# Kernel tuning notes

Hardware: AMD Instinct MI355X
Metric: run time of the kernel (lower is better)

Reference implementation:

```python
import jax, jax.numpy as jnp
import numpy as np

GAMMA = 1.0        # softmin temperature
BANDWIDTH = 0      # 0 => no Sakoe-Chiba band (numba code only skips when 0 < bw < |i-j|)
BIG = 1e30         # finite stand-in for +inf: exp(-BIG/gamma) underflows to exactly 0 in fp32,
                   # reproducing the inf-initialized R/SigR softmin ratios without NaNs
B, N, M = 32, 512, 512


def setup_inputs() -> dict:
    k1, k2 = jax.random.split(jax.random.key(0))
    D = jax.random.uniform(k1, (B, N, M), dtype=jnp.float32)    # pairwise distances (>= 0)
    Sig = jax.random.uniform(k2, (B, N, M), dtype=jnp.float32)  # per-cell uncertainty
    return {"D": D, "Sig": Sig}


def _soft_dtw(D, Sig):
    """uDTW forward DP (compute_softdtw), vectorized over anti-diagonal wavefronts.
    Returns jnp.stack([R[:, N, M], SigR[:, N, M]]) of shape (2, B)."""
    b, n, m = D.shape
    alpha = 1.0 / GAMMA
    # Dp[i, j] == D_new[i, j] = D[i-1, j-1] with zero border (indices 0..N, 0..M)
    Dp = jnp.pad(D, ((0, 0), (1, 0), (1, 0)))
    Sp = jnp.pad(Sig, ((0, 0), (1, 0), (1, 0)))
    iarr = jnp.arange(n + 1)

    def diag(A, d):
        # A[:, i, d - i] for i = 0..N, zero where j out of [0, M]
        j = d - iarr
        vals = A[:, iarr, jnp.clip(j, 0, m)]
        return jnp.where((j >= 0) & (j <= m), vals, 0.0)

    def shift(x, fill):
        # x[:, i-1] (index i-1 along the diagonal buffer)
        return jnp.concatenate([jnp.full((b, 1), fill, x.dtype), x[:, :-1]], axis=1)

    # diagonal buffers indexed by i; diag d=0 holds R[0,0]=0, rest inf(BIG); diag d=1 all inf
    r2 = jnp.full((b, n + 1), BIG, jnp.float32).at[:, 0].set(0.0)
    r1 = jnp.full((b, n + 1), BIG, jnp.float32)
    s2 = jnp.full((b, n + 1), BIG, jnp.float32).at[:, 0].set(0.0)
    s1 = jnp.full((b, n + 1), BIG, jnp.float32)

    def step(carry, d):
        r2, r1, s2, s1 = carry  # R/SigR diagonals d-2 and d-1
        j = d - iarr
        valid = (iarr >= 1) & (j >= 1) & (j <= m)
        if BANDWIDTH > 0:
            valid = valid & (jnp.abs(iarr - j) <= BANDWIDTH)
        # softmin ratios from R neighbors: (i-1,j-1)=prev2 shifted, (i-1,j)=prev1 shifted, (i,j-1)=prev1
        rr0 = -alpha * shift(r2, BIG)
        rr1 = -alpha * shift(r1, BIG)
        rr2 = -alpha * r1
        rmax = jnp.maximum(jnp.maximum(rr0, rr1), rr2)
        e0 = jnp.exp(rr0 - rmax)
        e1 = jnp.exp(rr1 - rmax)
        e2 = jnp.exp(rr2 - rmax)
        inv = 1.0 / (e0 + e1 + e2)
        p0, p1, p2 = e0 * inv, e1 * inv, e2 * inv
        dDd, dD1, dD2 = diag(Dp, d), diag(Dp, d - 1), diag(Dp, d - 2)
        dSd, dS1, dS2 = diag(Sp, d), diag(Sp, d - 1), diag(Sp, d - 2)
        # R[i,j] = D[i-1,j-1] + softmin-weighted avg of D_new neighbors (uDTW recurrence)
        newR = jnp.where(valid, dDd + p0 * shift(dD2, 0.0) + p1 * shift(dD1, 0.0) + p2 * dD1, BIG)
        newS = jnp.where(valid, dSd + p0 * shift(dS2, 0.0) + p1 * shift(dS1, 0.0) + p2 * dS1, BIG)
        return (r1, newR, s1, newS), None

    (_, rlast, _, slast), _ = jax.lax.scan(step, (r2, r1, s2, s1), jnp.arange(2, n + m + 1))
    # last anti-diagonal d = N + M contains cell (N, M) at index i = N
    return jnp.stack([rlast[:, n], slast[:, n]])  # (2, B)


def reference(D, Sig):
    return _soft_dtw(D, Sig)
```

## Files before the change

### kernel.cpp

```cpp
#include <hip/hip_runtime.h>


constexpr int N = 512;
constexpr int M = 512;
constexpr int BATCH = 32;
constexpr int NM = N + M;
constexpr int K = 32;
constexpr int NB = 32;
constexpr int PHASES = NB + 7;
constexpr float NL2E = -1.4426950408889634f;
constexpr float NLN2 = -0.6931471805599453f;
constexpr float EPS  = 1e-30f;

__device__ __forceinline__ float lane_shr1_or(float oldv, float x) {
  return __int_as_float(__builtin_amdgcn_update_dpp(
      __float_as_int(oldv), __float_as_int(x), 0x138, 0xf, 0xf, false));
}
__device__ __forceinline__ int qclamp(int q) {
  return q < 0 ? 0 : (q > 127 ? 127 : q);
}

__global__ __launch_bounds__(512, 2)
void softdtw_fwd(const float* __restrict__ D,
                 const float* __restrict__ Sig,
                 float* __restrict__ out) {
  const int b = blockIdx.x;
  const int t = threadIdx.x;
  const int w = t >> 6;
  const float4* Drow4 = (const float4*)(D + ((size_t)b * N + t) * M);

  __shared__ float2 edge[8][640];
  for (int idx = t; idx < 8 * 640; idx += 512)
    ((float2*)edge)[idx] = make_float2(0.f, 0.f);

  float eSelf = 0.f, dSelfL = 0.f;
  float eN2 = (t == 0) ? 1.f : 0.f, dN2L = 0.f;

  float sgA = 0.f, sg0 = 0.f, sg1 = 0.f, sg2 = 0.f;
  if (t == N - 1) {
    const float* Sb = Sig + (size_t)b * N * M;
    sgA = Sb[(size_t)(N - 1) * M + (M - 1)];
    sg0 = Sb[(size_t)(N - 2) * M + (M - 2)];
    sg1 = Sb[(size_t)(N - 2) * M + (M - 1)];
    sg2 = Sb[(size_t)(N - 1) * M + (M - 2)];
  }

  const int Bl = 2 * w, Bh = 2 * w + 17;

  float4 r0, r1, r2, r3, r4, r5, r6, r7, r8;
  {
    const int q = (32 * Bl - t) >> 2;
    r0 = Drow4[qclamp(q + 0)]; r1 = Drow4[qclamp(q + 1)];
    r2 = Drow4[qclamp(q + 2)]; r3 = Drow4[qclamp(q + 3)];
    r4 = Drow4[qclamp(q + 4)]; r5 = Drow4[qclamp(q + 5)];
    r6 = Drow4[qclamp(q + 6)]; r7 = Drow4[qclamp(q + 7)];
    r8 = Drow4[qclamp(q + 8)];
  }
  __syncthreads();

  for (int p = 0; p < PHASES; ++p) {
    const int B = p - w;
    const int nB = B + 1;
    const bool dopre = (nB >= Bl) && (nB <= Bh);

    float4 p0, p1, p2, p3, p4, p5, p6, p7, p8;
    if (dopre) {
      const int q = (32 * nB - t) >> 2;
      p0 = Drow4[qclamp(q + 0)]; p1 = Drow4[qclamp(q + 1)];
      p2 = Drow4[qclamp(q + 2)]; p3 = Drow4[qclamp(q + 3)];
      p4 = Drow4[qclamp(q + 4)]; p5 = Drow4[qclamp(q + 5)];
      p6 = Drow4[qclamp(q + 6)]; p7 = Drow4[qclamp(q + 7)];
      p8 = Drow4[qclamp(q + 8)];
    }

    if (B >= Bl && B <= Bh) {
      const int d0 = 2 + B * K;
      const int c0 = d0 - t - 2;

      float4 n0, n1, n2, n3, n4, n5, n6, n7, n8, n9, n10, n11, n12, n13, n14, n15;
      if (w > 0) {
        const float4* ep = (const float4*)&edge[w - 1][64 + (d0 - 64 * w - 2)];
        n0 = ep[0];  n1 = ep[1];  n2 = ep[2];  n3 = ep[3];
        n4 = ep[4];  n5 = ep[5];  n6 = ep[6];  n7 = ep[7];
        n8 = ep[8];  n9 = ep[9];  n10 = ep[10]; n11 = ep[11];
        n12 = ep[12]; n13 = ep[13]; n14 = ep[14]; n15 = ep[15];
      } else {
        const float4 z = make_float4(0.f, 0.f, 0.f, 0.f);
        n0 = n1 = n2 = n3 = n4 = n5 = n6 = n7 = z;
        n8 = n9 = n10 = n11 = n12 = n13 = n14 = n15 = z;
      }

      const int s = c0 & 3;
      const bool s2 = (s & 2) != 0, s1b = (s & 1) != 0;
      const float
        f0 = r0.x, f1 = r0.y, f2 = r0.z, f3 = r0.w,
        f4 = r1.x, f5 = r1.y, f6 = r1.z, f7 = r1.w,
        f8 = r2.x, f9 = r2.y, f10 = r2.z, f11 = r2.w,
        f12 = r3.x, f13 = r3.y, f14 = r3.z, f15 = r3.w,
        f16 = r4.x, f17 = r4.y, f18 = r4.z, f19 = r4.w,
        f20 = r5.x, f21 = r5.y, f22 = r5.z, f23 = r5.w,
        f24 = r6.x, f25 = r6.y, f26 = r6.z, f27 = r6.w,
        f28 = r7.x, f29 = r7.y, f30 = r7.z, f31 = r7.w,
        f32 = r8.x, f33 = r8.y, f34 = r8.z, f35 = r8.w;
      const float
        x0  = s2 ? f2  : f0,  x1  = s2 ? f3  : f1,  x2  = s2 ? f4  : f2,
        x3  = s2 ? f5  : f3,  x4  = s2 ? f6  : f4,  x5  = s2 ? f7  : f5,
        x6  = s2 ? f8  : f6,  x7  = s2 ? f9  : f7,  x8  = s2 ? f10 : f8,
        x9  = s2 ? f11 : f9,  x10 = s2 ? f12 : f10, x11 = s2 ? f13 : f11,
        x12 = s2 ? f14 : f12, x13 = s2 ? f15 : f13, x14 = s2 ? f16 : f14,
        x15 = s2 ? f17 : f15, x16 = s2 ? f18 : f16, x17 = s2 ? f19 : f17,
        x18 = s2 ? f20 : f18, x19 = s2 ? f21 : f19, x20 = s2 ? f22 : f20,
        x21 = s2 ? f23 : f21, x22 = s2 ? f24 : f22, x23 = s2 ? f25 : f23,
        x24 = s2 ? f26 : f24, x25 = s2 ? f27 : f25, x26 = s2 ? f28 : f26,
        x27 = s2 ? f29 : f27, x28 = s2 ? f30 : f28, x29 = s2 ? f31 : f29,
        x30 = s2 ? f32 : f30, x31 = s2 ? f33 : f31, x32 = s2 ? f34 : f32;
      const float
        g0  = s1b ? x1  : x0,  g1  = s1b ? x2  : x1,  g2  = s1b ? x3  : x2,
        g3  = s1b ? x4  : x3,  g4  = s1b ? x5  : x4,  g5  = s1b ? x6  : x5,
        g6  = s1b ? x7  : x6,  g7  = s1b ? x8  : x7,  g8  = s1b ? x9  : x8,
        g9  = s1b ? x10 : x9,  g10 = s1b ? x11 : x10, g11 = s1b ? x12 : x11,
        g12 = s1b ? x13 : x12, g13 = s1b ? x14 : x13, g14 = s1b ? x15 : x14,
        g15 = s1b ? x16 : x15, g16 = s1b ? x17 : x16, g17 = s1b ? x18 : x17,
        g18 = s1b ? x19 : x18, g19 = s1b ? x20 : x19, g20 = s1b ? x21 : x20,
        g21 = s1b ? x22 : x21, g22 = s1b ? x23 : x22, g23 = s1b ? x24 : x23,
        g24 = s1b ? x25 : x24, g25 = s1b ? x26 : x25, g26 = s1b ? x27 : x26,
        g27 = s1b ? x28 : x27, g28 = s1b ? x29 : x28, g29 = s1b ? x30 : x29,
        g30 = s1b ? x31 : x30, g31 = s1b ? x32 : x31;

      float2* eput = &edge[w][64 + c0];

#define STEP(kk, GK, NE, ND)                                                   \
      {                                                                        \
        const int c = c0 + (kk);                                               \
        const bool valid = ((unsigned)c) < 512u;                               \
        const float ddL = (GK) * NL2E;                                         \
        const float ddLm = valid ? ddL : -1e30f;                               \
        const float sE = lane_shr1_or((NE), eSelf);                            \
        const float sD = lane_shr1_or((ND), dSelfL);                           \
        const float e0 = eN2, e2 = eSelf;                                      \
        const float s02 = (e0 + e2) + EPS;                                     \
        const float sum = s02 + sE;                                            \
        const float inv = __builtin_amdgcn_rcpf(sum);                          \
        const float numL = fmaf(e0, dN2L, fmaf(sE, sD, e2 * dSelfL));          \
        const float rr = fmaf(inv, numL, ddLm);                                \
        const float newE = __builtin_amdgcn_exp2f(rr);                         \
        if (d0 + (kk) == NM && t == N - 1) {                                   \
          out[b] = rr * NLN2;                                                  \
          out[BATCH + b] = sgA + inv * (e0 * sg0 + sE * sg1 + e2 * sg2);       \
        }                                                                      \
        eN2 = sE; dN2L = sD;                                                   \
        eSelf = newE; dSelfL = ddL;                                            \
        eput[kk] = make_float2(newE, ddL);                                     \
      }
#define STEP2(m, GA, GB)                                                       \
      STEP(2 * m, GA, n##m.x, n##m.y)                                          \
      STEP(2 * m + 1, GB, n##m.z, n##m.w)

      STEP2(0,  g0,  g1)   STEP2(1,  g2,  g3)
      STEP2(2,  g4,  g5)   STEP2(3,  g6,  g7)
      STEP2(4,  g8,  g9)   STEP2(5,  g10, g11)
      STEP2(6,  g12, g13)  STEP2(7,  g14, g15)
      STEP2(8,  g16, g17)  STEP2(9,  g18, g19)
      STEP2(10, g20, g21)  STEP2(11, g22, g23)
      STEP2(12, g24, g25)  STEP2(13, g26, g27)
      STEP2(14, g28, g29)  STEP2(15, g30, g31)
#undef STEP2
#undef STEP
    }

    if (dopre) {
      r0 = p0; r1 = p1; r2 = p2; r3 = p3; r4 = p4;
      r5 = p5; r6 = p6; r7 = p7; r8 = p8;
    }
    __syncthreads();
  }
}

extern "C" void kernel_launch(void* const* d_in, const int* in_sizes, int n_in,
                              void* d_out, int out_size, void* d_ws, size_t ws_size,
                              hipStream_t stream) {
  const float* D   = (const float*)d_in[0];
  const float* Sig = (const float*)d_in[1];
  float* out = (float*)d_out;
  softdtw_fwd<<<dim3(BATCH), dim3(512), 0, stream>>>(D, Sig, out);
}
```

Baseline: 179.9 us.

## Process two DP rows per thread with 256-thread blocks and split edge buffers

Each thread now owns two adjacent rows of the DP grid, so a block of 256 threads (4 waves) covers all 512 rows. Row B consumes row A's values from the same step in registers rather than through cross-lane or shared-memory exchange. This halves the number of waves chained along the wavefront and cuts the phase count, reducing barrier rounds and pipeline fill. In exchange each thread has twice as much serial work per step, needs about twice the registers for the prefetched D rows, and the shared edge buffer is split into separate E and D arrays.

```diff
diff --git a/kernel.cpp b/kernel.cpp
--- a/kernel.cpp
+++ b/kernel.cpp
@@ -7,7 +7,7 @@
 constexpr int NM = N + M;
 constexpr int K = 32;
 constexpr int NB = 32;
-constexpr int PHASES = NB + 7;
+constexpr int PHASES = NB + 3;
 constexpr float NL2E = -1.4426950408889634f;
 constexpr float NLN2 = -0.6931471805599453f;
 constexpr float EPS  = 1e-30f;
@@ -20,24 +20,31 @@
   return q < 0 ? 0 : (q > 127 ? 127 : q);
 }
 
-__global__ __launch_bounds__(512, 2)
+__global__ __launch_bounds__(256, 1)
 void softdtw_fwd(const float* __restrict__ D,
                  const float* __restrict__ Sig,
                  float* __restrict__ out) {
   const int b = blockIdx.x;
   const int t = threadIdx.x;
   const int w = t >> 6;
-  const float4* Drow4 = (const float4*)(D + ((size_t)b * N + t) * M);
-
-  __shared__ float2 edge[8][640];
-  for (int idx = t; idx < 8 * 640; idx += 512)
-    ((float2*)edge)[idx] = make_float2(0.f, 0.f);
-
-  float eSelf = 0.f, dSelfL = 0.f;
-  float eN2 = (t == 0) ? 1.f : 0.f, dN2L = 0.f;
+  const float4* DrowA4 = (const float4*)(D + ((size_t)b * N + 2 * t) * M);
+  const float4* DrowB4 = (const float4*)(D + ((size_t)b * N + 2 * t + 1) * M);
+
+  __shared__ float edgeE[4][768];
+  __shared__ float edgeD[4][768];
+  for (int idx = t; idx < 4 * 768; idx += 256) {
+    (&edgeE[0][0])[idx] = 0.f;
+    (&edgeD[0][0])[idx] = 0.f;
+  }
+
+  float eSelfA = 0.f, dSelfA = 0.f;
+  float eA1 = 0.f, dA1 = 0.f;
+  float eN2A = (t == 0) ? 1.f : 0.f;
+  float dN2A = 0.f;
+  float eSelfB = 0.f, dSelfB = 0.f;
 
   float sgA = 0.f, sg0 = 0.f, sg1 = 0.f, sg2 = 0.f;
-  if (t == N - 1) {
+  if (t == 255) {
     const float* Sb = Sig + (size_t)b * N * M;
     sgA = Sb[(size_t)(N - 1) * M + (M - 1)];
     sg0 = Sb[(size_t)(N - 2) * M + (M - 2)];
@@ -45,16 +52,25 @@
     sg2 = Sb[(size_t)(N - 1) * M + (M - 2)];
   }
 
-  const int Bl = 2 * w, Bh = 2 * w + 17;
-
-  float4 r0, r1, r2, r3, r4, r5, r6, r7, r8;
+  const int Bl = 4 * w, Bh = 4 * w + 19;
+  const bool sA2 = (t & 1) != 0;
+  const bool sB2 = (t & 1) == 0;
+
+  float4 u0,u1,u2,u3,u4,u5,u6,u7,u8;
+  float4 v0,v1,v2,v3,v4,v5,v6,v7,v8;
   {
-    const int q = (32 * Bl - t) >> 2;
-    r0 = Drow4[qclamp(q + 0)]; r1 = Drow4[qclamp(q + 1)];
-    r2 = Drow4[qclamp(q + 2)]; r3 = Drow4[qclamp(q + 3)];
-    r4 = Drow4[qclamp(q + 4)]; r5 = Drow4[qclamp(q + 5)];
-    r6 = Drow4[qclamp(q + 6)]; r7 = Drow4[qclamp(q + 7)];
-    r8 = Drow4[qclamp(q + 8)];
+    const int qa = (32 * Bl - 2 * t) >> 2;
+    u0 = DrowA4[qclamp(qa + 0)]; u1 = DrowA4[qclamp(qa + 1)];
+    u2 = DrowA4[qclamp(qa + 2)]; u3 = DrowA4[qclamp(qa + 3)];
+    u4 = DrowA4[qclamp(qa + 4)]; u5 = DrowA4[qclamp(qa + 5)];
+    u6 = DrowA4[qclamp(qa + 6)]; u7 = DrowA4[qclamp(qa + 7)];
+    u8 = DrowA4[qclamp(qa + 8)];
+    const int qb = (32 * Bl - 2 * t - 1) >> 2;
+    v0 = DrowB4[qclamp(qb + 0)]; v1 = DrowB4[qclamp(qb + 1)];
+    v2 = DrowB4[qclamp(qb + 2)]; v3 = DrowB4[qclamp(qb + 3)];
+    v4 = DrowB4[qclamp(qb + 4)]; v5 = DrowB4[qclamp(qb + 5)];
+    v6 = DrowB4[qclamp(qb + 6)]; v7 = DrowB4[qclamp(qb + 7)];
+    v8 = DrowB4[qclamp(qb + 8)];
   }
   __syncthreads();
 
@@ -63,114 +79,151 @@
     const int nB = B + 1;
     const bool dopre = (nB >= Bl) && (nB <= Bh);
 
-    float4 p0, p1, p2, p3, p4, p5, p6, p7, p8;
+    float4 pu0,pu1,pu2,pu3,pu4,pu5,pu6,pu7,pu8;
+    float4 pv0,pv1,pv2,pv3,pv4,pv5,pv6,pv7,pv8;
     if (dopre) {
-      const int q = (32 * nB - t) >> 2;
-      p0 = Drow4[qclamp(q + 0)]; p1 = Drow4[qclamp(q + 1)];
-      p2 = Drow4[qclamp(q + 2)]; p3 = Drow4[qclamp(q + 3)];
-      p4 = Drow4[qclamp(q + 4)]; p5 = Drow4[qclamp(q + 5)];
-      p6 = Drow4[qclamp(q + 6)]; p7 = Drow4[qclamp(q + 7)];
-      p8 = Drow4[qclamp(q + 8)];
+      const int qa = (32 * nB - 2 * t) >> 2;
+      pu0 = DrowA4[qclamp(qa + 0)]; pu1 = DrowA4[qclamp(qa + 1)];
+      pu2 = DrowA4[qclamp(qa + 2)]; pu3 = DrowA4[qclamp(qa + 3)];
+      pu4 = DrowA4[qclamp(qa + 4)]; pu5 = DrowA4[qclamp(qa + 5)];
+      pu6 = DrowA4[qclamp(qa + 6)]; pu7 = DrowA4[qclamp(qa + 7)];
+      pu8 = DrowA4[qclamp(qa + 8)];
+      const int qb = (32 * nB - 2 * t - 1) >> 2;
+      pv0 = DrowB4[qclamp(qb + 0)]; pv1 = DrowB4[qclamp(qb + 1)];
+      pv2 = DrowB4[qclamp(qb + 2)]; pv3 = DrowB4[qclamp(qb + 3)];
+      pv4 = DrowB4[qclamp(qb + 4)]; pv5 = DrowB4[qclamp(qb + 5)];
+      pv6 = DrowB4[qclamp(qb + 6)]; pv7 = DrowB4[qclamp(qb + 7)];
+      pv8 = DrowB4[qclamp(qb + 8)];
     }
 
     if (B >= Bl && B <= Bh) {
       const int d0 = 2 + B * K;
-      const int c0 = d0 - t - 2;
-
-      float4 n0, n1, n2, n3, n4, n5, n6, n7, n8, n9, n10, n11, n12, n13, n14, n15;
+      const int cA0 = 32 * B - 2 * t;
+
+      float4 nE0,nE1,nE2,nE3,nE4,nE5,nE6,nE7;
+      float4 nD0,nD1,nD2,nD3,nD4,nD5,nD6,nD7;
       if (w > 0) {
-        const float4* ep = (const float4*)&edge[w - 1][64 + (d0 - 64 * w - 2)];
-        n0 = ep[0];  n1 = ep[1];  n2 = ep[2];  n3 = ep[3];
-        n4 = ep[4];  n5 = ep[5];  n6 = ep[6];  n7 = ep[7];
-        n8 = ep[8];  n9 = ep[9];  n10 = ep[10]; n11 = ep[11];
-        n12 = ep[12]; n13 = ep[13]; n14 = ep[14]; n15 = ep[15];
+        const int ebase = 32 * B - 128 * w + 128;
+        const float4* epE = (const float4*)&edgeE[w - 1][ebase];
+        const float4* epD = (const float4*)&edgeD[w - 1][ebase];
+        nE0 = epE[0]; nE1 = epE[1]; nE2 = epE[2]; nE3 = epE[3];
+        nE4 = epE[4]; nE5 = epE[5]; nE6 = epE[6]; nE7 = epE[7];
+        nD0 = epD[0]; nD1 = epD[1]; nD2 = epD[2]; nD3 = epD[3];
+        nD4 = epD[4]; nD5 = epD[5]; nD6 = epD[6]; nD7 = epD[7];
       } else {
         const float4 z = make_float4(0.f, 0.f, 0.f, 0.f);
-        n0 = n1 = n2 = n3 = n4 = n5 = n6 = n7 = z;
-        n8 = n9 = n10 = n11 = n12 = n13 = n14 = n15 = z;
+        nE0=z;nE1=z;nE2=z;nE3=z;nE4=z;nE5=z;nE6=z;nE7=z;
+        nD0=z;nD1=z;nD2=z;nD3=z;nD4=z;nD5=z;nD6=z;nD7=z;
       }
 
-      const int s = c0 & 3;
-      const bool s2 = (s & 2) != 0, s1b = (s & 1) != 0;
-      const float
-        f0 = r0.x, f1 = r0.y, f2 = r0.z, f3 = r0.w,
-        f4 = r1.x, f5 = r1.y, f6 = r1.z, f7 = r1.w,
-        f8 = r2.x, f9 = r2.y, f10 = r2.z, f11 = r2.w,
-        f12 = r3.x, f13 = r3.y, f14 = r3.z, f15 = r3.w,
-        f16 = r4.x, f17 = r4.y, f18 = r4.z, f19 = r4.w,
-        f20 = r5.x, f21 = r5.y, f22 = r5.z, f23 = r5.w,
-        f24 = r6.x, f25 = r6.y, f26 = r6.z, f27 = r6.w,
-        f28 = r7.x, f29 = r7.y, f30 = r7.z, f31 = r7.w,
-        f32 = r8.x, f33 = r8.y, f34 = r8.z, f35 = r8.w;
-      const float
-        x0  = s2 ? f2  : f0,  x1  = s2 ? f3  : f1,  x2  = s2 ? f4  : f2,
-        x3  = s2 ? f5  : f3,  x4  = s2 ? f6  : f4,  x5  = s2 ? f7  : f5,
-        x6  = s2 ? f8  : f6,  x7  = s2 ? f9  : f7,  x8  = s2 ? f10 : f8,
-        x9  = s2 ? f11 : f9,  x10 = s2 ? f12 : f10, x11 = s2 ? f13 : f11,
-        x12 = s2 ? f14 : f12, x13 = s2 ? f15 : f13, x14 = s2 ? f16 : f14,
-        x15 = s2 ? f17 : f15, x16 = s2 ? f18 : f16, x17 = s2 ? f19 : f17,
-        x18 = s2 ? f20 : f18, x19 = s2 ? f21 : f19, x20 = s2 ? f22 : f20,
-        x21 = s2 ? f23 : f21, x22 = s2 ? f24 : f22, x23 = s2 ? f25 : f23,
-        x24 = s2 ? f26 : f24, x25 = s2 ? f27 : f25, x26 = s2 ? f28 : f26,
-        x27 = s2 ? f29 : f27, x28 = s2 ? f30 : f28, x29 = s2 ? f31 : f29,
-        x30 = s2 ? f32 : f30, x31 = s2 ? f33 : f31, x32 = s2 ? f34 : f32;
-      const float
-        g0  = s1b ? x1  : x0,  g1  = s1b ? x2  : x1,  g2  = s1b ? x3  : x2,
-        g3  = s1b ? x4  : x3,  g4  = s1b ? x5  : x4,  g5  = s1b ? x6  : x5,
-        g6  = s1b ? x7  : x6,  g7  = s1b ? x8  : x7,  g8  = s1b ? x9  : x8,
-        g9  = s1b ? x10 : x9,  g10 = s1b ? x11 : x10, g11 = s1b ? x12 : x11,
-        g12 = s1b ? x13 : x12, g13 = s1b ? x14 : x13, g14 = s1b ? x15 : x14,
-        g15 = s1b ? x16 : x15, g16 = s1b ? x17 : x16, g17 = s1b ? x18 : x17,
-        g18 = s1b ? x19 : x18, g19 = s1b ? x20 : x19, g20 = s1b ? x21 : x20,
-        g21 = s1b ? x22 : x21, g22 = s1b ? x23 : x22, g23 = s1b ? x24 : x23,
-        g24 = s1b ? x25 : x24, g25 = s1b ? x26 : x25, g26 = s1b ? x27 : x26,
-        g27 = s1b ? x28 : x27, g28 = s1b ? x29 : x28, g29 = s1b ? x30 : x29,
-        g30 = s1b ? x31 : x30, g31 = s1b ? x32 : x31;
-
-      float2* eput = &edge[w][64 + c0];
-
-#define STEP(kk, GK, NE, ND)                                                   \
-      {                                                                        \
-        const int c = c0 + (kk);                                               \
-        const bool valid = ((unsigned)c) < 512u;                               \
-        const float ddL = (GK) * NL2E;                                         \
-        const float ddLm = valid ? ddL : -1e30f;                               \
-        const float sE = lane_shr1_or((NE), eSelf);                            \
-        const float sD = lane_shr1_or((ND), dSelfL);                           \
-        const float e0 = eN2, e2 = eSelf;                                      \
-        const float s02 = (e0 + e2) + EPS;                                     \
-        const float sum = s02 + sE;                                            \
-        const float inv = __builtin_amdgcn_rcpf(sum);                          \
-        const float numL = fmaf(e0, dN2L, fmaf(sE, sD, e2 * dSelfL));          \
-        const float rr = fmaf(inv, numL, ddLm);                                \
-        const float newE = __builtin_amdgcn_exp2f(rr);                         \
-        if (d0 + (kk) == NM && t == N - 1) {                                   \
-          out[b] = rr * NLN2;                                                  \
-          out[BATCH + b] = sgA + inv * (e0 * sg0 + sE * sg1 + e2 * sg2);       \
-        }                                                                      \
-        eN2 = sE; dN2L = sD;                                                   \
-        eSelf = newE; dSelfL = ddL;                                            \
-        eput[kk] = make_float2(newE, ddL);                                     \
+      const float
+        A0=u0.x, A1=u0.y, A2=u0.z, A3=u0.w,  A4=u1.x, A5=u1.y, A6=u1.z, A7=u1.w,
+        A8=u2.x, A9=u2.y, A10=u2.z, A11=u2.w, A12=u3.x, A13=u3.y, A14=u3.z, A15=u3.w,
+        A16=u4.x, A17=u4.y, A18=u4.z, A19=u4.w, A20=u5.x, A21=u5.y, A22=u5.z, A23=u5.w,
+        A24=u6.x, A25=u6.y, A26=u6.z, A27=u6.w, A28=u7.x, A29=u7.y, A30=u7.z, A31=u7.w,
+        A32=u8.x, A33=u8.y;
+      const float
+        F1=v0.y, F2=v0.z, F3=v0.w,  F4=v1.x, F5=v1.y, F6=v1.z, F7=v1.w,
+        F8=v2.x, F9=v2.y, F10=v2.z, F11=v2.w, F12=v3.x, F13=v3.y, F14=v3.z, F15=v3.w,
+        F16=v4.x, F17=v4.y, F18=v4.z, F19=v4.w, F20=v5.x, F21=v5.y, F22=v5.z, F23=v5.w,
+        F24=v6.x, F25=v6.y, F26=v6.z, F27=v6.w, F28=v7.x, F29=v7.y, F30=v7.z, F31=v7.w,
+        F32=v8.x, F33=v8.y, F34=v8.z;
+
+      const float
+        gA0 =sA2?A2 :A0,  gA1 =sA2?A3 :A1,  gA2 =sA2?A4 :A2,  gA3 =sA2?A5 :A3,
+        gA4 =sA2?A6 :A4,  gA5 =sA2?A7 :A5,  gA6 =sA2?A8 :A6,  gA7 =sA2?A9 :A7,
+        gA8 =sA2?A10:A8,  gA9 =sA2?A11:A9,  gA10=sA2?A12:A10, gA11=sA2?A13:A11,
+        gA12=sA2?A14:A12, gA13=sA2?A15:A13, gA14=sA2?A16:A14, gA15=sA2?A17:A15,
+        gA16=sA2?A18:A16, gA17=sA2?A19:A17, gA18=sA2?A20:A18, gA19=sA2?A21:A19,
+        gA20=sA2?A22:A20, gA21=sA2?A23:A21, gA22=sA2?A24:A22, gA23=sA2?A25:A23,
+        gA24=sA2?A26:A24, gA25=sA2?A27:A25, gA26=sA2?A28:A26, gA27=sA2?A29:A27,
+        gA28=sA2?A30:A28, gA29=sA2?A31:A29, gA30=sA2?A32:A30, gA31=sA2?A33:A31;
+      const float
+        gB0 =sB2?F3 :F1,  gB1 =sB2?F4 :F2,  gB2 =sB2?F5 :F3,  gB3 =sB2?F6 :F4,
+        gB4 =sB2?F7 :F5,  gB5 =sB2?F8 :F6,  gB6 =sB2?F9 :F7,  gB7 =sB2?F10:F8,
+        gB8 =sB2?F11:F9,  gB9 =sB2?F12:F10, gB10=sB2?F13:F11, gB11=sB2?F14:F12,
+        gB12=sB2?F15:F13, gB13=sB2?F16:F14, gB14=sB2?F17:F15, gB15=sB2?F18:F16,
+        gB16=sB2?F19:F17, gB17=sB2?F20:F18, gB18=sB2?F21:F19, gB19=sB2?F22:F20,
+        gB20=sB2?F23:F21, gB21=sB2?F24:F22, gB22=sB2?F25:F23, gB23=sB2?F26:F24,
+        gB24=sB2?F27:F25, gB25=sB2?F28:F26, gB26=sB2?F29:F27, gB27=sB2?F30:F28,
+        gB28=sB2?F31:F29, gB29=sB2?F32:F30, gB30=sB2?F33:F31, gB31=sB2?F34:F32;
+
+      float* pE = &edgeE[w][128 + cA0 - 1];
+      float* pD = &edgeD[w][128 + cA0 - 1];
+
+#define STEP(kk, NEv, NDv, GA, GB)                                            \
+      {                                                                       \
+        const float eA0v = eSelfA, dA0v = dSelfA;                             \
+        const float eB0v = eSelfB, dB0v = dSelfB;                             \
+        const int cA = cA0 + (kk);                                            \
+        const float ddLA = (GA) * NL2E;                                       \
+        const float ddLAm = ((unsigned)cA < 512u) ? ddLA : -1e30f;            \
+        const float ddLB = (GB) * NL2E;                                       \
+        const float ddLBm = ((unsigned)(cA - 1) < 512u) ? ddLB : -1e30f;      \
+        const float sEA = lane_shr1_or((NEv), eB0v);                          \
+        const float sDA = lane_shr1_or((NDv), dB0v);                          \
+        const float sumA = ((eN2A + eA0v) + EPS) + sEA;                       \
+        const float invA = __builtin_amdgcn_rcpf(sumA);                       \
+        const float numA = fmaf(eN2A, dN2A, fmaf(sEA, sDA, eA0v * dA0v));     \
+        const float rrA = fmaf(invA, numA, ddLAm);                            \
+        const float newEA = __builtin_amdgcn_exp2f(rrA);                      \
+        const float sumB = ((eA1 + eB0v) + EPS) + eA0v;                       \
+        const float invB = __builtin_amdgcn_rcpf(sumB);                       \
+        const float numB = fmaf(eA1, dA1, fmaf(eA0v, dA0v, eB0v * dB0v));     \
+        const float rrB = fmaf(invB, numB, ddLBm);                            \
+        const float newEB = __builtin_amdgcn_exp2f(rrB);                      \
+        if (d0 + (kk) == NM && t == 255) {                                    \
+          out[b] = rrB * NLN2;                                                \
+          out[BATCH + b] = sgA + invB * (eA1 * sg0 + eA0v * sg1 + eB0v * sg2);\
+        }                                                                     \
+        eN2A = sEA; dN2A = sDA;                                               \
+        eA1 = eA0v; dA1 = dA0v;                                               \
+        eSelfA = newEA; dSelfA = ddLA;                                        \
+        eSelfB = newEB; dSelfB = ddLB;                                        \
+        pE[kk] = newEB;                                                       \
+        pD[kk] = ddLB;                                                        \
       }
-#define STEP2(m, GA, GB)                                                       \
-      STEP(2 * m, GA, n##m.x, n##m.y)                                          \
-      STEP(2 * m + 1, GB, n##m.z, n##m.w)
-
-      STEP2(0,  g0,  g1)   STEP2(1,  g2,  g3)
-      STEP2(2,  g4,  g5)   STEP2(3,  g6,  g7)
-      STEP2(4,  g8,  g9)   STEP2(5,  g10, g11)
-      STEP2(6,  g12, g13)  STEP2(7,  g14, g15)
-      STEP2(8,  g16, g17)  STEP2(9,  g18, g19)
-      STEP2(10, g20, g21)  STEP2(11, g22, g23)
-      STEP2(12, g24, g25)  STEP2(13, g26, g27)
-      STEP2(14, g28, g29)  STEP2(15, g30, g31)
-#undef STEP2
+
+      STEP(0,  nE0.x, nD0.x, gA0,  gB0)
+      STEP(1,  nE0.y, nD0.y, gA1,  gB1)
+      STEP(2,  nE0.z, nD0.z, gA2,  gB2)
+      STEP(3,  nE0.w, nD0.w, gA3,  gB3)
+      STEP(4,  nE1.x, nD1.x, gA4,  gB4)
+      STEP(5,  nE1.y, nD1.y, gA5,  gB5)
+      STEP(6,  nE1.z, nD1.z, gA6,  gB6)
+      STEP(7,  nE1.w, nD1.w, gA7,  gB7)
+      STEP(8,  nE2.x, nD2.x, gA8,  gB8)
+      STEP(9,  nE2.y, nD2.y, gA9,  gB9)
+      STEP(10, nE2.z, nD2.z, gA10, gB10)
+      STEP(11, nE2.w, nD2.w, gA11, gB11)
+      STEP(12, nE3.x, nD3.x, gA12, gB12)
+      STEP(13, nE3.y, nD3.y, gA13, gB13)
+      STEP(14, nE3.z, nD3.z, gA14, gB14)
+      STEP(15, nE3.w, nD3.w, gA15, gB15)
+      STEP(16, nE4.x, nD4.x, gA16, gB16)
+      STEP(17, nE4.y, nD4.y, gA17, gB17)
+      STEP(18, nE4.z, nD4.z, gA18, gB18)
+      STEP(19, nE4.w, nD4.w, gA19, gB19)
+      STEP(20, nE5.x, nD5.x, gA20, gB20)
+      STEP(21, nE5.y, nD5.y, gA21, gB21)
+      STEP(22, nE5.z, nD5.z, gA22, gB22)
+      STEP(23, nE5.w, nD5.w, gA23, gB23)
+      STEP(24, nE6.x, nD6.x, gA24, gB24)
+      STEP(25, nE6.y, nD6.y, gA25, gB25)
+      STEP(26, nE6.z, nD6.z, gA26, gB26)
+      STEP(27, nE6.w, nD6.w, gA27, gB27)
+      STEP(28, nE7.x, nD7.x, gA28, gB28)
+      STEP(29, nE7.y, nD7.y, gA29, gB29)
+      STEP(30, nE7.z, nD7.z, gA30, gB30)
+      STEP(31, nE7.w, nD7.w, gA31, gB31)
 #undef STEP
     }
 
     if (dopre) {
-      r0 = p0; r1 = p1; r2 = p2; r3 = p3; r4 = p4;
-      r5 = p5; r6 = p6; r7 = p7; r8 = p8;
+      u0 = pu0; u1 = pu1; u2 = pu2; u3 = pu3; u4 = pu4;
+      u5 = pu5; u6 = pu6; u7 = pu7; u8 = pu8;
+      v0 = pv0; v1 = pv1; v2 = pv2; v3 = pv3; v4 = pv4;
+      v5 = pv5; v6 = pv6; v7 = pv7; v8 = pv8;
     }
     __syncthreads();
   }
@@ -182,5 +235,5 @@
   const float* D   = (const float*)d_in[0];
   const float* Sig = (const float*)d_in[1];
   float* out = (float*)d_out;
-  softdtw_fwd<<<dim3(BATCH), dim3(512), 0, stream>>>(D, Sig, out);
-}
+  softdtw_fwd<<<dim3(BATCH), dim3(256), 0, stream>>>(D, Sig, out);
+}
```

Result: slower. 202.8 us (+12.7%).
